# Kernel tuning notes

Measured on AMD Instinct MI355X. Metric: run time of the kernel, lower is better.

Reference implementation:

```python
import jax, jax.numpy as jnp
import numpy as np

B, F, G, L, C = 32768, 512, 16, 64, 1000  # batch, feature_dim, n_groups, labels/group, num_classes


def setup_inputs() -> dict:
    key = jax.random.key(0)
    k1, k2, k3, k4, k5 = jax.random.split(key, 5)
    features = jax.random.normal(k1, (B, F), dtype=jnp.float32)
    group_probs = jax.random.uniform(k2, (B, G), dtype=jnp.float32)
    # stacked per-group Linear heads: W[g] is the (L, F) weight of head g, b[g] its bias
    W = jax.random.normal(k3, (G, L, F), dtype=jnp.float32) / np.sqrt(F).astype(np.float32)
    b = jax.random.normal(k4, (G, L), dtype=jnp.float32) * 0.01
    # group_to_labels: label_ids[g, j] = shared class id that head g's j-th output maps to
    label_ids = jax.random.randint(k5, (G, L), 0, C, dtype=jnp.int32)
    return {"features": features, "group_probs": group_probs, "W": W, "b": b,
            "label_ids": label_ids}


def reference(features, group_probs, W, b, label_ids):
    # all per-group linear heads as one batched GEMM: [B,G,L]
    group_logits = jnp.einsum('bf,glf->bgl', features, W) + b
    # weight each group's logits by its group probability
    weighted = group_probs[:, :, None] * group_logits          # [B, G, L]
    # scatter-add into the shared logit tensor (duplicate class ids accumulate)
    flat_idx = label_ids.reshape(-1)                            # [G*L]
    logits = jnp.zeros((features.shape[0], C), dtype=features.dtype)
    logits = logits.at[:, flat_idx].add(weighted.reshape(features.shape[0], -1))
    return logits
```

## Files before the change

### kernel.cpp

```cpp
#include <hip/hip_runtime.h>
#include <stdint.h>

#define B_SZ   32768
#define F_SZ   512
#define G_SZ   16
#define L_SZ   64
#define N_COLS 1024
#define C_SZ   1000
#define M_TILE 64
#define A_STRIDE 520
#define W_STRIDE 1042
#define SMEM_BYTES 66688

typedef __attribute__((ext_vector_type(8))) short short8;
typedef __attribute__((ext_vector_type(4))) float floatx4;

__device__ __forceinline__ unsigned short f2bf(float f) {
    unsigned int x = __float_as_uint(f);
    x += 0x7fffu + ((x >> 16) & 1u);
    return (unsigned short)(x >> 16);
}

__global__ __launch_bounds__(1024) void build_csr_kernel(const int* __restrict__ label_ids,
                                                         const float* __restrict__ bias,
                                                         int* __restrict__ off,
                                                         int* __restrict__ list,
                                                         float* __restrict__ bias_p,
                                                         unsigned char* __restrict__ g_perm) {
    __shared__ int cnt[1024];
    __shared__ int cur[1024];
    const int t = threadIdx.x;
    cnt[t] = 0;
    __syncthreads();
    const int lbl = label_ids[t];
    atomicAdd(&cnt[lbl], 1);
    __syncthreads();
    int v = cnt[t];
    #pragma unroll
    for (int d = 1; d < 1024; d <<= 1) {
        int u = (t >= d) ? cnt[t - d] : 0;
        __syncthreads();
        v += u;
        cnt[t] = v;
        __syncthreads();
    }
    int ex = (t == 0) ? 0 : cnt[t - 1];
    cur[t] = ex;
    if (t <= C_SZ) off[t] = (t == 0) ? 0 : cnt[t - 1];
    __syncthreads();
    int pos = atomicAdd(&cur[lbl], 1);
    list[pos]   = t;
    bias_p[pos] = bias[t];
    g_perm[pos] = (unsigned char)(t >> 6);
}

__global__ __launch_bounds__(256) void convert_w_kernel(const float* __restrict__ W,
                                                        const int* __restrict__ list,
                                                        unsigned short* __restrict__ Wb) {
    int idx = blockIdx.x * 256 + threadIdx.x;
    int row = idx >> 7;
    int c4  = idx & 127;
    int src = list[row];
    const float4* W4 = (const float4*)W;
    float4 v = W4[src * 128 + c4];
    ushort4 u = make_ushort4(f2bf(v.x), f2bf(v.y), f2bf(v.z), f2bf(v.w));
    ((ushort4*)Wb)[idx] = u;
}

__global__ __launch_bounds__(1024, 4) void mhc_main_kernel(
        const float* __restrict__ feat,
        const float* __restrict__ gp,
        const unsigned short* __restrict__ Wb,
        const float* __restrict__ bias_p,
        const int* __restrict__ off,
        const unsigned char* __restrict__ g_perm,
        float* __restrict__ out)
{
    __shared__ __align__(16) char smem[SMEM_BYTES];
    __shared__ float gp_s[M_TILE * G_SZ];
    __shared__ float bias_s[N_COLS];
    __shared__ unsigned char g_s[N_COLS];

    unsigned short* As = (unsigned short*)smem;
    float* WL = (float*)smem;

    const int t    = threadIdx.x;
    const int wave = t >> 6;
    const int lane = t & 63;
    const int m16  = lane & 15;
    const int quad = lane >> 4;
    const int r0   = blockIdx.x * M_TILE;

    gp_s[t]   = gp[r0 * G_SZ + t];
    bias_s[t] = bias_p[t];
    g_s[t]    = g_perm[t];

    int e0 = 0, e1 = 0;
    if (t < C_SZ) { e0 = off[t]; e1 = off[t + 1]; }

    {
        const float4* f4 = (const float4*)(feat + (size_t)r0 * F_SZ);
        #pragma unroll
        for (int i = 0; i < 8; ++i) {
            int idx = t + i * 1024;
            int row = idx >> 7;
            int c4  = idx & 127;
            float4 v = f4[idx];
            ushort4 u = make_ushort4(f2bf(v.x), f2bf(v.y), f2bf(v.z), f2bf(v.w));
            *(ushort4*)(As + row * A_STRIDE + c4 * 4) = u;
        }
    }
    __syncthreads();

    const floatx4 zero = {0.f, 0.f, 0.f, 0.f};
    floatx4 acc[4][4];
    #pragma unroll
    for (int i = 0; i < 4; ++i)
        #pragma unroll
        for (int j = 0; j < 4; ++j) acc[i][j] = zero;

    const unsigned short* aBase = As + m16 * A_STRIDE + quad * 8;
    const unsigned short* bBase = Wb + (size_t)(wave * 64 + m16) * F_SZ + quad * 8;

    #pragma unroll 4
    for (int kt = 0; kt < 16; ++kt) {
        short8 a[4];
        #pragma unroll
        for (int rt = 0; rt < 4; ++rt)
            a[rt] = *(const short8*)(aBase + rt * 16 * A_STRIDE + kt * 32);
        #pragma unroll
        for (int ct = 0; ct < 4; ++ct) {
            short8 b = *(const short8*)(bBase + ct * 16 * F_SZ + kt * 32);
            #pragma unroll
            for (int rt = 0; rt < 4; ++rt)
                acc[rt][ct] = __builtin_amdgcn_mfma_f32_16x16x32_bf16(a[rt], b, acc[rt][ct], 0, 0, 0);
        }
    }

    #pragma unroll
    for (int p = 0; p < 4; ++p) {
        __syncthreads();
        #pragma unroll
        for (int ct = 0; ct < 4; ++ct) {
            int col = wave * 64 + ct * 16 + m16;
            int g   = g_s[col];
            float bi = bias_s[col];
            #pragma unroll
            for (int r = 0; r < 4; ++r) {
                int rl = quad * 4 + r;
                float v = gp_s[(p * 16 + rl) * G_SZ + g] * (acc[p][ct][r] + bi);
                WL[rl * W_STRIDE + col] = v;
            }
        }
        __syncthreads();
        if (t < C_SZ) {
            #pragma unroll
            for (int h = 0; h < 4; ++h) {
                float s0 = 0.f, s1 = 0.f, s2 = 0.f, s3 = 0.f;
                for (int j = e0; j < e1; ++j) {
                    s0 += WL[(h * 4 + 0) * W_STRIDE + j];
                    s1 += WL[(h * 4 + 1) * W_STRIDE + j];
                    s2 += WL[(h * 4 + 2) * W_STRIDE + j];
                    s3 += WL[(h * 4 + 3) * W_STRIDE + j];
                }
                size_t rowg = (size_t)(r0 + p * 16 + h * 4);
                out[(rowg + 0) * C_SZ + t] = s0;
                out[(rowg + 1) * C_SZ + t] = s1;
                out[(rowg + 2) * C_SZ + t] = s2;
                out[(rowg + 3) * C_SZ + t] = s3;
            }
        }
    }
}

extern "C" void kernel_launch(void* const* d_in, const int* in_sizes, int n_in,
                              void* d_out, int out_size, void* d_ws, size_t ws_size,
                              hipStream_t stream) {
    const float* feat  = (const float*)d_in[0];
    const float* gp    = (const float*)d_in[1];
    const float* W     = (const float*)d_in[2];
    const float* bias  = (const float*)d_in[3];
    const int* labels  = (const int*)d_in[4];
    float* out = (float*)d_out;

    unsigned short* Wb = (unsigned short*)d_ws;
    char* base = (char*)d_ws + (1 << 20);
    int* off             = (int*)base;
    int* list            = (int*)(base + 4096);
    float* bias_p        = (float*)(base + 8192);
    unsigned char* g_prm = (unsigned char*)(base + 12288);

    build_csr_kernel<<<1, 1024, 0, stream>>>(labels, bias, off, list, bias_p, g_prm);
    convert_w_kernel<<<(N_COLS * F_SZ / 4) / 256, 256, 0, stream>>>(W, list, Wb);
    mhc_main_kernel<<<B_SZ / M_TILE, 1024, 0, stream>>>(feat, gp, Wb, bias_p, off, g_prm, out);
}
```

Measured before the change: 257.0 us.

## Halve row tile, transpose weighted-logit staging with swizzle, nontemporal IO

Halves the row tile per block to 32 and raises the occupancy hint from 4 to 8 blocks. Reshapes the shared staging of weighted logits into a column-major layout, 16 rows per column, with an XOR swizzle. This lets each class thread gather all 16 rows of a contributing column with vector loads instead of strided scalar reads. The feature reads and the output writes become nontemporal to avoid polluting the cache. The trade is more blocks, each reloading the bf16 weights and bias/group tables, against better LDS access and higher occupancy.

```diff
diff --git a/kernel.cpp b/kernel.cpp
--- a/kernel.cpp
+++ b/kernel.cpp
@@ -7,10 +7,9 @@
 #define L_SZ   64
 #define N_COLS 1024
 #define C_SZ   1000
-#define M_TILE 64
+#define M_TILE 32
 #define A_STRIDE 520
-#define W_STRIDE 1042
-#define SMEM_BYTES 66688
+#define SMEM_BYTES 65536
 
 typedef __attribute__((ext_vector_type(8))) short short8;
 typedef __attribute__((ext_vector_type(4))) float floatx4;
@@ -67,7 +66,7 @@
     ((ushort4*)Wb)[idx] = u;
 }
 
-__global__ __launch_bounds__(1024, 4) void mhc_main_kernel(
+__global__ __launch_bounds__(1024, 8) void mhc_main_kernel(
         const float* __restrict__ feat,
         const float* __restrict__ gp,
         const unsigned short* __restrict__ Wb,
@@ -82,7 +81,7 @@
     __shared__ unsigned char g_s[N_COLS];
 
     unsigned short* As = (unsigned short*)smem;
-    float* WL = (float*)smem;
+    float* WT = (float*)smem;
 
     const int t    = threadIdx.x;
     const int wave = t >> 6;
@@ -91,84 +90,87 @@
     const int quad = lane >> 4;
     const int r0   = blockIdx.x * M_TILE;
 
-    gp_s[t]   = gp[r0 * G_SZ + t];
+    if (t < M_TILE * G_SZ) gp_s[t] = gp[r0 * G_SZ + t];
     bias_s[t] = bias_p[t];
     g_s[t]    = g_perm[t];
 
-    int e0 = 0, e1 = 0;
-    if (t < C_SZ) { e0 = off[t]; e1 = off[t + 1]; }
-
     {
-        const float4* f4 = (const float4*)(feat + (size_t)r0 * F_SZ);
+        const floatx4* f4 = (const floatx4*)(feat + (size_t)r0 * F_SZ);
         #pragma unroll
-        for (int i = 0; i < 8; ++i) {
+        for (int i = 0; i < 4; ++i) {
             int idx = t + i * 1024;
             int row = idx >> 7;
             int c4  = idx & 127;
-            float4 v = f4[idx];
-            ushort4 u = make_ushort4(f2bf(v.x), f2bf(v.y), f2bf(v.z), f2bf(v.w));
+            floatx4 v = __builtin_nontemporal_load(f4 + idx);
+            ushort4 u = make_ushort4(f2bf(v[0]), f2bf(v[1]), f2bf(v[2]), f2bf(v[3]));
             *(ushort4*)(As + row * A_STRIDE + c4 * 4) = u;
         }
     }
     __syncthreads();
 
     const floatx4 zero = {0.f, 0.f, 0.f, 0.f};
-    floatx4 acc[4][4];
+    floatx4 acc[2][4];
     #pragma unroll
-    for (int i = 0; i < 4; ++i)
+    for (int i = 0; i < 2; ++i)
         #pragma unroll
         for (int j = 0; j < 4; ++j) acc[i][j] = zero;
 
     const unsigned short* aBase = As + m16 * A_STRIDE + quad * 8;
     const unsigned short* bBase = Wb + (size_t)(wave * 64 + m16) * F_SZ + quad * 8;
 
-    #pragma unroll 4
+    #pragma unroll 2
     for (int kt = 0; kt < 16; ++kt) {
-        short8 a[4];
-        #pragma unroll
-        for (int rt = 0; rt < 4; ++rt)
-            a[rt] = *(const short8*)(aBase + rt * 16 * A_STRIDE + kt * 32);
+        short8 a0 = *(const short8*)(aBase + kt * 32);
+        short8 a1 = *(const short8*)(aBase + 16 * A_STRIDE + kt * 32);
         #pragma unroll
         for (int ct = 0; ct < 4; ++ct) {
             short8 b = *(const short8*)(bBase + ct * 16 * F_SZ + kt * 32);
-            #pragma unroll
-            for (int rt = 0; rt < 4; ++rt)
-                acc[rt][ct] = __builtin_amdgcn_mfma_f32_16x16x32_bf16(a[rt], b, acc[rt][ct], 0, 0, 0);
+            acc[0][ct] = __builtin_amdgcn_mfma_f32_16x16x32_bf16(a0, b, acc[0][ct], 0, 0, 0);
+            acc[1][ct] = __builtin_amdgcn_mfma_f32_16x16x32_bf16(a1, b, acc[1][ct], 0, 0, 0);
         }
     }
 
+    int e0 = 0, e1 = 0;
+    if (t < C_SZ) { e0 = off[t]; e1 = off[t + 1]; }
+
     #pragma unroll
-    for (int p = 0; p < 4; ++p) {
+    for (int p = 0; p < 2; ++p) {
         __syncthreads();
         #pragma unroll
         for (int ct = 0; ct < 4; ++ct) {
             int col = wave * 64 + ct * 16 + m16;
             int g   = g_s[col];
             float bi = bias_s[col];
+            int slot = quad ^ ((col ^ (col >> 2)) & 3);
+            floatx4 w;
             #pragma unroll
             for (int r = 0; r < 4; ++r) {
                 int rl = quad * 4 + r;
-                float v = gp_s[(p * 16 + rl) * G_SZ + g] * (acc[p][ct][r] + bi);
-                WL[rl * W_STRIDE + col] = v;
+                w[r] = gp_s[(p * 16 + rl) * G_SZ + g] * (acc[p][ct][r] + bi);
             }
+            *(floatx4*)(WT + col * 16 + slot * 4) = w;
         }
         __syncthreads();
         if (t < C_SZ) {
+            float s[16];
             #pragma unroll
-            for (int h = 0; h < 4; ++h) {
-                float s0 = 0.f, s1 = 0.f, s2 = 0.f, s3 = 0.f;
-                for (int j = e0; j < e1; ++j) {
-                    s0 += WL[(h * 4 + 0) * W_STRIDE + j];
-                    s1 += WL[(h * 4 + 1) * W_STRIDE + j];
-                    s2 += WL[(h * 4 + 2) * W_STRIDE + j];
-                    s3 += WL[(h * 4 + 3) * W_STRIDE + j];
+            for (int i = 0; i < 16; ++i) s[i] = 0.f;
+            for (int j = e0; j < e1; ++j) {
+                int sw = (j ^ (j >> 2)) & 3;
+                const float* cbase = WT + j * 16;
+                #pragma unroll
+                for (int q = 0; q < 4; ++q) {
+                    floatx4 v = *(const floatx4*)(cbase + ((q ^ sw) << 2));
+                    s[q * 4 + 0] += v[0];
+                    s[q * 4 + 1] += v[1];
+                    s[q * 4 + 2] += v[2];
+                    s[q * 4 + 3] += v[3];
                 }
-                size_t rowg = (size_t)(r0 + p * 16 + h * 4);
-                out[(rowg + 0) * C_SZ + t] = s0;
-                out[(rowg + 1) * C_SZ + t] = s1;
-                out[(rowg + 2) * C_SZ + t] = s2;
-                out[(rowg + 3) * C_SZ + t] = s3;
             }
+            size_t rowg = (size_t)(r0 + p * 16);
+            #pragma unroll
+            for (int rr = 0; rr < 16; ++rr)
+                __builtin_nontemporal_store(s[rr], out + (rowg + rr) * C_SZ + t);
         }
     }
 }
```

New measurement: 304.7 us. +18.6%, slower.
